# Kernel tuning notes

Measured on AMD Instinct MI355X. Metric: run time of the kernel, lower is better.

The kernel has to match this reference:

```python
import jax, jax.numpy as jnp
import numpy as np

B, S, D, H, HD = 2, 2048, 2048, 16, 128


def precompute_freqs_cis(dim, end, theta=10000.0):
    freqs = 1.0 / theta ** (np.arange(0, dim, 2, dtype=np.float32)[: dim // 2] / dim)
    t = np.arange(end, dtype=np.float32)
    freqs = np.outer(t, freqs)
    freqs = np.concatenate((freqs, freqs), axis=-1)  # [S, HD]
    return jnp.asarray(np.cos(freqs)), jnp.asarray(np.sin(freqs))


def rotate_half(x):
    x1, x2 = x[..., : x.shape[-1] // 2], x[..., x.shape[-1] // 2 :]
    return jnp.concatenate((-x2, x1), axis=-1)


def setup_inputs() -> dict:
    key = jax.random.key(0)
    ks = jax.random.split(key, 5)
    scale = 1.0 / np.sqrt(D)
    return {
        "x": jax.random.normal(ks[0], (B, S, D), jnp.float32),
        "mask": jnp.ones((1, 1, S, S), jnp.bool_),
        "Wq": jax.random.normal(ks[1], (D, H, HD), jnp.float32) * scale,
        "Wk": jax.random.normal(ks[2], (D, H, HD), jnp.float32) * scale,
        "Wv": jax.random.normal(ks[3], (D, H, HD), jnp.float32) * scale,
        "Wo": jax.random.normal(ks[4], (H, HD, D), jnp.float32) * scale,
    }


def reference(x, mask, Wq, Wk, Wv, Wo):
    seq_len = x.shape[1]
    head_dim = Wq.shape[-1]
    # QKV projections: [B,S,D] x [D,H,HD] -> [B,S,H,HD]
    q = jnp.einsum("bsd,dhk->bshk", x, Wq)
    k = jnp.einsum("bsd,dhk->bshk", x, Wk)
    v = jnp.einsum("bsd,dhk->bshk", x, Wv)
    # Rotary position embedding
    cos, sin = precompute_freqs_cis(head_dim, seq_len)
    cos = cos[None, :, None, :]  # [1,S,1,HD]
    sin = sin[None, :, None, :]
    q = q * cos + rotate_half(q) * sin
    k = k * cos + rotate_half(k) * sin
    # Scaled dot-product attention (flax dot_product_attention semantics)
    scores = jnp.einsum("bqhk,bskh->bhqs", q / jnp.sqrt(jnp.float32(head_dim)), k.swapaxes(-1, -2))
    big_neg = jnp.finfo(scores.dtype).min
    scores = jnp.where(mask, scores, big_neg)
    attn = jax.nn.softmax(scores, axis=-1)  # [B,H,S,S]
    ctx = jnp.einsum("bhqs,bshk->bqhk", attn, v)  # [B,S,H,HD]
    # Output projection over (head, head_dim)
    return jnp.einsum("bqhk,hkd->bqd", ctx, Wo)
```

## Files before the change

### kernel.cpp

```cpp
#include <hip/hip_runtime.h>
#include <math.h>

#define Bc   2
#define Sc   2048
#define Dc   2048
#define Hc   16
#define HDc  128
#define BSc  4096
#define HHDc 2048

typedef __bf16 bf16_t;
typedef __bf16 bf16x8 __attribute__((ext_vector_type(8)));
typedef __bf16 bf16x4 __attribute__((ext_vector_type(4)));
typedef float  f32x4  __attribute__((ext_vector_type(4)));

#define AS1(p) ((const __attribute__((address_space(1))) void*)(p))
#define AS3(p) ((__attribute__((address_space(3))) void*)(p))

#define MFMA16(a,b,c) __builtin_amdgcn_mfma_f32_16x16x32_bf16((a),(b),(c),0,0,0)

__global__ void convert_x(const float* __restrict__ x, bf16_t* __restrict__ xb)
{
    const size_t i = ((size_t)blockIdx.x * 256 + threadIdx.x) * 4;
    float4 v = *(const float4*)&x[i];
    bf16x4 o; o[0]=(bf16_t)v.x; o[1]=(bf16_t)v.y; o[2]=(bf16_t)v.z; o[3]=(bf16_t)v.w;
    *(bf16x4*)&xb[i] = o;
}

__global__ __launch_bounds__(256) void transpose_w(const float* __restrict__ in,
                                                   bf16_t* __restrict__ out)
{
    __shared__ float T[64][65];
    const int t = threadIdx.x;
    const int r0 = blockIdx.y * 64, c0 = blockIdx.x * 64;
    #pragma unroll
    for (int i = 0; i < 4; ++i) {
        int row = i * 16 + (t >> 4);
        int c4  = (t & 15) * 4;
        float4 v = *(const float4*)&in[(size_t)(r0 + row) * 2048 + c0 + c4];
        T[row][c4] = v.x; T[row][c4+1] = v.y; T[row][c4+2] = v.z; T[row][c4+3] = v.w;
    }
    __syncthreads();
    #pragma unroll
    for (int i = 0; i < 4; ++i) {
        int orow = i * 16 + (t >> 4);
        int c4   = (t & 15) * 4;
        bf16x4 o;
        #pragma unroll
        for (int j = 0; j < 4; ++j) o[j] = (bf16_t)T[c4 + j][orow];
        *(bf16x4*)&out[(size_t)(c0 + orow) * 2048 + r0 + c4] = o;
    }
}

__global__ __launch_bounds__(256) void prep_vtb(const bf16_t* __restrict__ V,
                                                bf16_t* __restrict__ Vt)
{
    __shared__ float T[64][65];
    const int t = threadIdx.x;
    const int s0 = blockIdx.x * 64;
    const int c0 = blockIdx.y * 64;
    const int bh = blockIdx.z;
    const int b = bh >> 4, h = bh & 15;
    #pragma unroll
    for (int i = 0; i < 4; ++i) {
        int row = i * 16 + (t >> 4);
        int c4  = (t & 15) * 4;
        bf16x4 v = *(const bf16x4*)&V[((size_t)(b * Sc + s0 + row)) * HHDc + h * HDc + c0 + c4];
        #pragma unroll
        for (int j = 0; j < 4; ++j) T[row][c4 + j] = (float)v[j];
    }
    __syncthreads();
    #pragma unroll
    for (int i = 0; i < 4; ++i) {
        int orow = i * 16 + (t >> 4);
        int c4   = (t & 15) * 4;
        bf16x4 o;
        #pragma unroll
        for (int j = 0; j < 4; ++j) o[j] = (bf16_t)T[c4 + j][orow];
        *(bf16x4*)&Vt[((size_t)bh * HDc + c0 + orow) * Sc + s0 + c4] = o;
    }
}

__global__ __launch_bounds__(256) void qkv_gemm(const bf16_t* __restrict__ A,
                                                const bf16_t* __restrict__ Bt,
                                                float* __restrict__ Qf,
                                                float* __restrict__ Kf,
                                                bf16_t* __restrict__ Vb)
{
    __shared__ bf16_t As[128 * 64];
    __shared__ bf16_t Bs[128 * 64];
    const int t = threadIdx.x;
    const int w = t >> 6, l = t & 63;
    const int wm = w >> 1, wn = w & 1;
    const int lane15 = l & 15, quad = l >> 4;
    const int swr = (lane15 & 7) * 8;

    const int id  = blockIdx.y * 48 + blockIdx.x;
    const int swz = (id & 7) * 192 + (id >> 3);
    const int m0 = (swz / 48) * 128, n0 = (swz % 48) * 128;

    f32x4 acc[4][4];
    #pragma unroll
    for (int i = 0; i < 4; ++i)
        #pragma unroll
        for (int j = 0; j < 4; ++j)
            #pragma unroll
            for (int c = 0; c < 4; ++c) acc[i][j][c] = 0.f;

    const int srow = w * 8 + (l >> 3);
    const int gk   = ((l & 7) * 8) ^ ((srow & 7) * 8);

    for (int k0 = 0; k0 < 2048; k0 += 64) {
        __syncthreads();
        #pragma unroll
        for (int p = 0; p < 4; ++p) {
            __builtin_amdgcn_global_load_lds(
                AS1(A + (size_t)(m0 + p * 32 + srow) * 2048 + k0 + gk),
                AS3(&As[(p * 32 + w * 8) * 64]), 16, 0, 0);
            __builtin_amdgcn_global_load_lds(
                AS1(Bt + (size_t)(n0 + p * 32 + srow) * 2048 + k0 + gk),
                AS3(&Bs[(p * 32 + w * 8) * 64]), 16, 0, 0);
        }
        __syncthreads();
        #pragma unroll
        for (int ks = 0; ks < 2; ++ks) {
            const int rc = ((ks * 4 + quad) * 8) ^ swr;
            bf16x8 a[4], b[4];
            #pragma unroll
            for (int mt = 0; mt < 4; ++mt)
                a[mt] = *(const bf16x8*)&As[(wm * 64 + mt * 16 + lane15) * 64 + rc];
            #pragma unroll
            for (int nt = 0; nt < 4; ++nt)
                b[nt] = *(const bf16x8*)&Bs[(wn * 64 + nt * 16 + lane15) * 64 + rc];
            #pragma unroll
            for (int mt = 0; mt < 4; ++mt)
                #pragma unroll
                for (int nt = 0; nt < 4; ++nt)
                    acc[mt][nt] = MFMA16(a[mt], b[nt], acc[mt][nt]);
        }
    }

    if (n0 < 4096) {
        float* __restrict__ dst = (n0 < 2048) ? Qf : Kf;
        const int nb = n0 & 2047;
        #pragma unroll
        for (int mt = 0; mt < 4; ++mt)
            #pragma unroll
            for (int nt = 0; nt < 4; ++nt)
                #pragma unroll
                for (int r = 0; r < 4; ++r) {
                    const int gm = m0 + wm * 64 + mt * 16 + quad * 4 + r;
                    const int gn = nb + wn * 64 + nt * 16 + lane15;
                    dst[(size_t)gm * 2048 + gn] = acc[mt][nt][r];
                }
    } else {
        const int nb = n0 - 4096;
        #pragma unroll
        for (int mt = 0; mt < 4; ++mt)
            #pragma unroll
            for (int nt = 0; nt < 4; ++nt)
                #pragma unroll
                for (int r = 0; r < 4; ++r) {
                    const int gm = m0 + wm * 64 + mt * 16 + quad * 4 + r;
                    const int gn = nb + wn * 64 + nt * 16 + lane15;
                    Vb[(size_t)gm * 2048 + gn] = (bf16_t)acc[mt][nt][r];
                }
    }
}

__global__ __launch_bounds__(256) void gemm_bt(const bf16_t* __restrict__ A,
                                               const bf16_t* __restrict__ Bt,
                                               float* __restrict__ C)
{
    __shared__ bf16_t As[128 * 64];
    __shared__ bf16_t Bs[128 * 64];
    const int t = threadIdx.x;
    const int w = t >> 6, l = t & 63;
    const int wm = w >> 1, wn = w & 1;
    const int lane15 = l & 15, quad = l >> 4;
    const int swr = (lane15 & 7) * 8;

    const int id  = blockIdx.y * 16 + blockIdx.x;
    const int swz = (id & 7) * 64 + (id >> 3);
    const int m0 = (swz / 16) * 128, n0 = (swz % 16) * 128;

    f32x4 acc[4][4];
    #pragma unroll
    for (int i = 0; i < 4; ++i)
        #pragma unroll
        for (int j = 0; j < 4; ++j)
            #pragma unroll
            for (int c = 0; c < 4; ++c) acc[i][j][c] = 0.f;

    const int srow = w * 8 + (l >> 3);
    const int gk   = ((l & 7) * 8) ^ ((srow & 7) * 8);

    for (int k0 = 0; k0 < 2048; k0 += 64) {
        __syncthreads();
        #pragma unroll
        for (int p = 0; p < 4; ++p) {
            __builtin_amdgcn_global_load_lds(
                AS1(A + (size_t)(m0 + p * 32 + srow) * 2048 + k0 + gk),
                AS3(&As[(p * 32 + w * 8) * 64]), 16, 0, 0);
            __builtin_amdgcn_global_load_lds(
                AS1(Bt + (size_t)(n0 + p * 32 + srow) * 2048 + k0 + gk),
                AS3(&Bs[(p * 32 + w * 8) * 64]), 16, 0, 0);
        }
        __syncthreads();
        #pragma unroll
        for (int ks = 0; ks < 2; ++ks) {
            const int rc = ((ks * 4 + quad) * 8) ^ swr;
            bf16x8 a[4], b[4];
            #pragma unroll
            for (int mt = 0; mt < 4; ++mt)
                a[mt] = *(const bf16x8*)&As[(wm * 64 + mt * 16 + lane15) * 64 + rc];
            #pragma unroll
            for (int nt = 0; nt < 4; ++nt)
                b[nt] = *(const bf16x8*)&Bs[(wn * 64 + nt * 16 + lane15) * 64 + rc];
            #pragma unroll
            for (int mt = 0; mt < 4; ++mt)
                #pragma unroll
                for (int nt = 0; nt < 4; ++nt)
                    acc[mt][nt] = MFMA16(a[mt], b[nt], acc[mt][nt]);
        }
    }

    #pragma unroll
    for (int mt = 0; mt < 4; ++mt)
        #pragma unroll
        for (int nt = 0; nt < 4; ++nt)
            #pragma unroll
            for (int r = 0; r < 4; ++r) {
                const int gm = m0 + wm * 64 + mt * 16 + quad * 4 + r;
                const int gn = n0 + wn * 64 + nt * 16 + lane15;
                C[(size_t)gm * 2048 + gn] = acc[mt][nt][r];
            }
}

__global__ void rope_scale_cast(const float* __restrict__ Qf,
                                const float* __restrict__ Kf,
                                bf16_t* __restrict__ Qh,
                                bf16_t* __restrict__ Kh)
{
    const int idx  = blockIdx.x * 256 + threadIdx.x;
    const int j4   = (idx & 15) * 4;
    const int h    = (idx >> 4) & (Hc - 1);
    const int sabs = idx >> 8;
    const int s    = sabs & (Sc - 1);
    const float QS = 0.08838834764831845f;

    const size_t base = (size_t)sabs * HHDc + (size_t)h * HDc + j4;
    float4 q1 = *(const float4*)&Qf[base];
    float4 q2 = *(const float4*)&Qf[base + 64];
    float4 k1 = *(const float4*)&Kf[base];
    float4 k2 = *(const float4*)&Kf[base + 64];

    bf16x4 qo1, qo2, ko1, ko2;
    #pragma unroll
    for (int c = 0; c < 4; ++c) {
        const float freq = expf(-(float)(j4 + c) * 0.14391156514261520f);
        const float ang  = (float)s * freq;
        float sn, cs;
        sincosf(ang, &sn, &cs);
        const float a = ((const float*)&q1)[c], bq = ((const float*)&q2)[c];
        const float x = ((const float*)&k1)[c], y  = ((const float*)&k2)[c];
        qo1[c] = (bf16_t)((a * cs - bq * sn) * QS);
        qo2[c] = (bf16_t)((bq * cs + a * sn) * QS);
        ko1[c] = (bf16_t)(x * cs - y * sn);
        ko2[c] = (bf16_t)(y * cs + x * sn);
    }
    *(bf16x4*)&Qh[base]      = qo1;
    *(bf16x4*)&Qh[base + 64] = qo2;
    *(bf16x4*)&Kh[base]      = ko1;
    *(bf16x4*)&Kh[base + 64] = ko2;
}

__global__ __launch_bounds__(512, 4) void attn_v7(const bf16_t* __restrict__ Q,
                                                  const bf16_t* __restrict__ K,
                                                  const bf16_t* __restrict__ Vt,
                                                  bf16_t* __restrict__ CTX)
{
    __shared__ bf16_t Ks[64 * 128];
    __shared__ bf16_t Vts[128 * 64];
    __shared__ bf16_t Ps[128 * 72];

    const int t = threadIdx.x, w = t >> 6, l = t & 63;
    const int lane15 = l & 15, quad = l >> 4;
    const int swr = (lane15 & 7) * 8;
    const int q0 = blockIdx.x * 128;
    const int b = blockIdx.y >> 4, h = blockIdx.y & 15;
    const size_t qbase = ((size_t)(b * Sc + q0)) * HHDc + h * HDc;
    const size_t vtb   = (size_t)blockIdx.y * HDc * Sc;
    const size_t kb0   = ((size_t)(b * Sc)) * HHDc + h * HDc;

    bf16x8 qf[4];
    #pragma unroll
    for (int ks = 0; ks < 4; ++ks)
        qf[ks] = *(const bf16x8*)&Q[qbase
            + (size_t)(w * 16 + lane15) * HHDc + (ks * 4 + quad) * 8];

    float m_ = -INFINITY, l_ = 0.f;

    f32x4 O[8];
    #pragma unroll
    for (int i = 0; i < 8; ++i)
        #pragma unroll
        for (int c = 0; c < 4; ++c) O[i][c] = 0.f;

    const int krow0 = w * 4 + (l >> 4);
    const int kgc   = lane15 * 8;
    const int vrow0 = w * 8 + (l >> 3);
    const int vgc   = (l & 7) * 8;

    bf16x8 kst[2], vst[2];
    #pragma unroll
    for (int p = 0; p < 2; ++p) {
        kst[p] = *(const bf16x8*)&K[kb0 + (size_t)(p * 32 + krow0) * HHDc + kgc];
        vst[p] = *(const bf16x8*)&Vt[vtb + (size_t)(p * 64 + vrow0) * Sc + vgc];
    }

    for (int kt = 0; kt < Sc / 64; ++kt) {
        __syncthreads();
        #pragma unroll
        for (int p = 0; p < 2; ++p) {
            const int rk = p * 32 + krow0;
            *(bf16x8*)&Ks[rk * 128 + (kgc ^ ((rk & 7) * 8))] = kst[p];
        }
        #pragma unroll
        for (int p = 0; p < 2; ++p) {
            const int rv = p * 64 + vrow0;
            *(bf16x8*)&Vts[rv * 64 + (vgc ^ ((rv & 7) * 8))] = vst[p];
        }
        if (kt + 1 < Sc / 64) {
            const size_t kbn = kb0 + (size_t)(kt + 1) * 64 * HHDc;
            #pragma unroll
            for (int p = 0; p < 2; ++p) {
                kst[p] = *(const bf16x8*)&K[kbn + (size_t)(p * 32 + krow0) * HHDc + kgc];
                vst[p] = *(const bf16x8*)&Vt[vtb + (size_t)(p * 64 + vrow0) * Sc
                                             + (kt + 1) * 64 + vgc];
            }
        }
        __syncthreads();

        f32x4 sc[4];
        #pragma unroll
        for (int j = 0; j < 4; ++j)
            #pragma unroll
            for (int c = 0; c < 4; ++c) sc[j][c] = 0.f;
        __builtin_amdgcn_s_setprio(1);
        #pragma unroll
        for (int ks = 0; ks < 4; ++ks) {
            const int rc = ((ks * 4 + quad) * 8) ^ swr;
            bf16x8 bk[4];
            #pragma unroll
            for (int nt = 0; nt < 4; ++nt)
                bk[nt] = *(const bf16x8*)&Ks[(nt * 16 + lane15) * 128 + rc];
            #pragma unroll
            for (int nt = 0; nt < 4; ++nt)
                sc[nt] = MFMA16(bk[nt], qf[ks], sc[nt]);
        }
        __builtin_amdgcn_s_setprio(0);

        {
            float tm = -INFINITY;
            #pragma unroll
            for (int nt = 0; nt < 4; ++nt)
                #pragma unroll
                for (int r = 0; r < 4; ++r) tm = fmaxf(tm, sc[nt][r]);
            tm = fmaxf(tm, __shfl_xor(tm, 16));
            tm = fmaxf(tm, __shfl_xor(tm, 32));
            const float mo = m_;
            const float mn = fmaxf(mo, tm);
            const float al = __expf(mo - mn);
            m_ = mn;
            float ts = 0.f;
            const int prow = (w * 16 + lane15) * 72;
            #pragma unroll
            for (int nt = 0; nt < 4; ++nt) {
                bf16x4 pw;
                #pragma unroll
                for (int r = 0; r < 4; ++r) {
                    const float p = __expf(sc[nt][r] - mn);
                    pw[r] = (bf16_t)p;
                    ts += p;
                }
                *(bf16x4*)&Ps[prow + nt * 16 + quad * 4] = pw;
            }
            ts += __shfl_xor(ts, 16);
            ts += __shfl_xor(ts, 32);
            l_ = l_ * al + ts;

            #pragma unroll
            for (int ht = 0; ht < 8; ++ht)
                #pragma unroll
                for (int c = 0; c < 4; ++c) O[ht][c] *= al;
        }

        __builtin_amdgcn_s_setprio(1);
        #pragma unroll
        for (int ks = 0; ks < 2; ++ks) {
            const int rcp = (ks * 4 + quad) * 8;
            const int rcv = rcp ^ swr;
            bf16x8 av[8];
            #pragma unroll
            for (int ht = 0; ht < 8; ++ht)
                av[ht] = *(const bf16x8*)&Vts[(ht * 16 + lane15) * 64 + rcv];
            bf16x8 bp = *(const bf16x8*)&Ps[(w * 16 + lane15) * 72 + rcp];
            #pragma unroll
            for (int ht = 0; ht < 8; ++ht)
                O[ht] = MFMA16(av[ht], bp, O[ht]);
        }
        __builtin_amdgcn_s_setprio(0);
    }

    {
        const float linv = 1.0f / l_;
        const int s = q0 + w * 16 + lane15;
        #pragma unroll
        for (int ht = 0; ht < 8; ++ht) {
            bf16x4 o;
            #pragma unroll
            for (int c = 0; c < 4; ++c) o[c] = (bf16_t)(O[ht][c] * linv);
            *(bf16x4*)&CTX[((size_t)(b * Sc + s)) * HHDc + h * HDc + ht * 16 + quad * 4] = o;
        }
    }
}

extern "C" void kernel_launch(void* const* d_in, const int* in_sizes, int n_in,
                              void* d_out, int out_size, void* d_ws, size_t ws_size,
                              hipStream_t stream)
{
    const float* x  = (const float*)d_in[0];
    const float* Wq = (const float*)d_in[2];
    const float* Wk = (const float*)d_in[3];
    const float* Wv = (const float*)d_in[4];
    const float* Wo = (const float*)d_in[5];
    float* out = (float*)d_out;

    bf16_t* W0  = (bf16_t*)d_ws;
    bf16_t* xb  = W0;
    bf16_t* WT3 = W0 + 8388608;
    bf16_t* WoT = W0 + 20971520;
    float*  Qf  = (float*)(W0 + 25165824);
    float*  Kf  = (float*)(W0 + 41943040);
    bf16_t* Vb  = W0 + 58720256;
    bf16_t* Kh  = W0;
    bf16_t* Qh  = W0 + 8388608;
    bf16_t* Vt  = W0 + 25165824;
    bf16_t* CTX = W0 + 41943040;

    dim3 tw(32, 32);

    convert_x<<<8192, 256, 0, stream>>>(x, xb);
    transpose_w<<<tw, 256, 0, stream>>>(Wq, WT3);
    transpose_w<<<tw, 256, 0, stream>>>(Wk, WT3 + 4194304);
    transpose_w<<<tw, 256, 0, stream>>>(Wv, WT3 + 8388608);
    transpose_w<<<tw, 256, 0, stream>>>(Wo, WoT);

    qkv_gemm<<<dim3(48, 32), 256, 0, stream>>>(xb, WT3, Qf, Kf, Vb);

    rope_scale_cast<<<4096, 256, 0, stream>>>(Qf, Kf, Qh, Kh);
    prep_vtb<<<dim3(32, 2, 32), 256, 0, stream>>>(Vb, Vt);

    attn_v7<<<dim3(16, 32), 512, 0, stream>>>(Qh, Kh, Vt, CTX);

    gemm_bt<<<dim3(16, 32), 256, 0, stream>>>(CTX, WoT, out);
}
```

Before: 441.3 us.

## Fuse V transpose into QKV GEMM epilogue and precompute RoPE table

The QKV GEMM epilogue now writes V directly in transposed per-head layout, which removes the separate prep_vtb transpose kernel and its extra round trip through memory. A small rope_tab kernel precomputes cos/sin into the output buffer, which serves as scratch before the final GEMM overwrites it, so the RoPE kernel no longer evaluates expf and sincosf per element. The block-index swizzle in both GEMMs is also removed in favour of plain row-major tile mapping, which may hurt L2 locality. The transposed V stores are 4-element strided writes that could coalesce poorly.

Measured after the change: 426.2 us. -3.4%, faster.

```diff
diff --git a/kernel.cpp b/kernel.cpp
--- a/kernel.cpp
+++ b/kernel.cpp
@@ -52,40 +52,22 @@
     }
 }
 
-__global__ __launch_bounds__(256) void prep_vtb(const bf16_t* __restrict__ V,
-                                                bf16_t* __restrict__ Vt)
-{
-    __shared__ float T[64][65];
-    const int t = threadIdx.x;
-    const int s0 = blockIdx.x * 64;
-    const int c0 = blockIdx.y * 64;
-    const int bh = blockIdx.z;
-    const int b = bh >> 4, h = bh & 15;
-    #pragma unroll
-    for (int i = 0; i < 4; ++i) {
-        int row = i * 16 + (t >> 4);
-        int c4  = (t & 15) * 4;
-        bf16x4 v = *(const bf16x4*)&V[((size_t)(b * Sc + s0 + row)) * HHDc + h * HDc + c0 + c4];
-        #pragma unroll
-        for (int j = 0; j < 4; ++j) T[row][c4 + j] = (float)v[j];
-    }
-    __syncthreads();
-    #pragma unroll
-    for (int i = 0; i < 4; ++i) {
-        int orow = i * 16 + (t >> 4);
-        int c4   = (t & 15) * 4;
-        bf16x4 o;
-        #pragma unroll
-        for (int j = 0; j < 4; ++j) o[j] = (bf16_t)T[c4 + j][orow];
-        *(bf16x4*)&Vt[((size_t)bh * HDc + c0 + orow) * Sc + s0 + c4] = o;
-    }
+__global__ void rope_tab(float* __restrict__ tab)
+{
+    const int i = blockIdx.x * 256 + threadIdx.x;
+    const int j = i & 63, s = i >> 6;
+    const float freq = expf(-(float)j * 0.14391156514261520f);
+    float sn, cs;
+    sincosf((float)s * freq, &sn, &cs);
+    float2 v; v.x = cs; v.y = sn;
+    *(float2*)&tab[i * 2] = v;
 }
 
 __global__ __launch_bounds__(256) void qkv_gemm(const bf16_t* __restrict__ A,
                                                 const bf16_t* __restrict__ Bt,
                                                 float* __restrict__ Qf,
                                                 float* __restrict__ Kf,
-                                                bf16_t* __restrict__ Vb)
+                                                bf16_t* __restrict__ Vt)
 {
     __shared__ bf16_t As[128 * 64];
     __shared__ bf16_t Bs[128 * 64];
@@ -94,10 +76,7 @@
     const int wm = w >> 1, wn = w & 1;
     const int lane15 = l & 15, quad = l >> 4;
     const int swr = (lane15 & 7) * 8;
-
-    const int id  = blockIdx.y * 48 + blockIdx.x;
-    const int swz = (id & 7) * 192 + (id >> 3);
-    const int m0 = (swz / 48) * 128, n0 = (swz % 48) * 128;
+    const int m0 = blockIdx.y * 128, n0 = blockIdx.x * 128;
 
     f32x4 acc[4][4];
     #pragma unroll
@@ -156,15 +135,20 @@
     } else {
         const int nb = n0 - 4096;
         #pragma unroll
-        for (int mt = 0; mt < 4; ++mt)
-            #pragma unroll
-            for (int nt = 0; nt < 4; ++nt)
-                #pragma unroll
-                for (int r = 0; r < 4; ++r) {
-                    const int gm = m0 + wm * 64 + mt * 16 + quad * 4 + r;
-                    const int gn = nb + wn * 64 + nt * 16 + lane15;
-                    Vb[(size_t)gm * 2048 + gn] = (bf16_t)acc[mt][nt][r];
-                }
+        for (int mt = 0; mt < 4; ++mt) {
+            const int gm = m0 + wm * 64 + mt * 16 + quad * 4;
+            const int bq = gm >> 11;
+            const int s  = gm & 2047;
+            #pragma unroll
+            for (int nt = 0; nt < 4; ++nt) {
+                const int gn = nb + wn * 64 + nt * 16 + lane15;
+                const int h  = gn >> 7, hd = gn & 127;
+                bf16x4 o;
+                #pragma unroll
+                for (int r = 0; r < 4; ++r) o[r] = (bf16_t)acc[mt][nt][r];
+                *(bf16x4*)&Vt[((size_t)((bq * Hc + h) * HDc + hd)) * Sc + s] = o;
+            }
+        }
     }
 }
 
@@ -179,10 +163,7 @@
     const int wm = w >> 1, wn = w & 1;
     const int lane15 = l & 15, quad = l >> 4;
     const int swr = (lane15 & 7) * 8;
-
-    const int id  = blockIdx.y * 16 + blockIdx.x;
-    const int swz = (id & 7) * 64 + (id >> 3);
-    const int m0 = (swz / 16) * 128, n0 = (swz % 16) * 128;
+    const int m0 = blockIdx.y * 128, n0 = blockIdx.x * 128;
 
     f32x4 acc[4][4];
     #pragma unroll
@@ -239,6 +220,7 @@
 
 __global__ void rope_scale_cast(const float* __restrict__ Qf,
                                 const float* __restrict__ Kf,
+                                const float* __restrict__ tab,
                                 bf16_t* __restrict__ Qh,
                                 bf16_t* __restrict__ Kh)
 {
@@ -254,14 +236,14 @@
     float4 q2 = *(const float4*)&Qf[base + 64];
     float4 k1 = *(const float4*)&Kf[base];
     float4 k2 = *(const float4*)&Kf[base + 64];
+    float4 t0 = *(const float4*)&tab[(s * 64 + j4) * 2];
+    float4 t1 = *(const float4*)&tab[(s * 64 + j4 + 2) * 2];
 
     bf16x4 qo1, qo2, ko1, ko2;
     #pragma unroll
     for (int c = 0; c < 4; ++c) {
-        const float freq = expf(-(float)(j4 + c) * 0.14391156514261520f);
-        const float ang  = (float)s * freq;
-        float sn, cs;
-        sincosf(ang, &sn, &cs);
+        const float cs = (c < 2) ? ((c & 1) ? t0.z : t0.x) : ((c & 1) ? t1.z : t1.x);
+        const float sn = (c < 2) ? ((c & 1) ? t0.w : t0.y) : ((c & 1) ? t1.w : t1.y);
         const float a = ((const float*)&q1)[c], bq = ((const float*)&q2)[c];
         const float x = ((const float*)&k1)[c], y  = ((const float*)&k2)[c];
         qo1[c] = (bf16_t)((a * cs - bq * sn) * QS);
@@ -443,24 +425,24 @@
     bf16_t* WoT = W0 + 20971520;
     float*  Qf  = (float*)(W0 + 25165824);
     float*  Kf  = (float*)(W0 + 41943040);
-    bf16_t* Vb  = W0 + 58720256;
+    bf16_t* Vt  = W0 + 58720256;
     bf16_t* Kh  = W0;
     bf16_t* Qh  = W0 + 8388608;
-    bf16_t* Vt  = W0 + 25165824;
-    bf16_t* CTX = W0 + 41943040;
+    bf16_t* CTX = W0 + 25165824;
+    float*  tab = out;
 
     dim3 tw(32, 32);
 
+    rope_tab<<<512, 256, 0, stream>>>(tab);
     convert_x<<<8192, 256, 0, stream>>>(x, xb);
     transpose_w<<<tw, 256, 0, stream>>>(Wq, WT3);
     transpose_w<<<tw, 256, 0, stream>>>(Wk, WT3 + 4194304);
     transpose_w<<<tw, 256, 0, stream>>>(Wv, WT3 + 8388608);
     transpose_w<<<tw, 256, 0, stream>>>(Wo, WoT);
 
-    qkv_gemm<<<dim3(48, 32), 256, 0, stream>>>(xb, WT3, Qf, Kf, Vb);
-
-    rope_scale_cast<<<4096, 256, 0, stream>>>(Qf, Kf, Qh, Kh);
-    prep_vtb<<<dim3(32, 2, 32), 256, 0, stream>>>(Vb, Vt);
+    qkv_gemm<<<dim3(48, 32), 256, 0, stream>>>(xb, WT3, Qf, Kf, Vt);
+
+    rope_scale_cast<<<4096, 256, 0, stream>>>(Qf, Kf, tab, Qh, Kh);
 
     attn_v7<<<dim3(16, 32), 512, 0, stream>>>(Qh, Kh, Vt, CTX);
 
```
